# Performance work log

Measured on AMD Instinct MI355X. Metric: run time of the kernel, lower is better.

The kernel has to match this reference:

```python
import jax, jax.numpy as jnp
import numpy as np

D_M, L_OBS, ALPHA, D_H, D_V, N_HEADS = 64, 256, 256, 256, 64, 8


def setup_inputs():
    key = jax.random.key(0)
    ks = jax.random.split(key, 18)
    x_ts = jax.random.normal(ks[0], (D_M, L_OBS), dtype=jnp.float32)
    t_raw = jax.random.uniform(ks[1], (D_M, L_OBS), dtype=jnp.float32) * ALPHA
    drop = jax.random.uniform(ks[2], (D_M, L_OBS)) < 0.5
    t_ts = jnp.where(drop, -1.0, t_raw)  # negative time == invalid observation
    global_means = jax.random.normal(ks[3], (D_M,), dtype=jnp.float32)
    s = 0.05
    return {
        'x_ts': x_ts, 't_ts': t_ts, 'global_means': global_means,
        'conv_w': jax.random.normal(ks[4], (D_H, D_M)) * s,
        'conv_b': jax.random.normal(ks[5], (D_H,)) * s,
        't2v_w': jax.random.normal(ks[6], (N_HEADS, D_V)),
        't2v_phi': jax.random.normal(ks[7], (N_HEADS, D_V)),
        'wq_w': jax.random.normal(ks[8], (N_HEADS, D_V, D_V)) * s,
        'wq_b': jax.random.normal(ks[9], (N_HEADS, D_V)) * s,
        'wk_w': jax.random.normal(ks[10], (N_HEADS, D_V, D_V)) * s,
        'wk_b': jax.random.normal(ks[11], (N_HEADS, D_V)) * s,
        'proj_w': jax.random.normal(ks[12], (D_H, N_HEADS)) * s,
        'proj_b': jax.random.normal(ks[13], (D_H,)) * s,
        'g1_w': jax.random.normal(ks[14], (D_H, 2 * D_H)) * s,
        'g1_b': jax.random.normal(ks[15], (D_H,)) * s,
        'g2_w': jax.random.normal(ks[16], (D_H, D_H)) * s,
        'g2_b': jax.random.normal(ks[17], (D_H,)) * s,
    }


def _time2vec(tau, w, phi):
    # tau [...], w/phi [H, D_V] -> [H, *tau.shape, D_V]; dim 0 linear, rest sin
    shp = (N_HEADS,) + (1,) * tau.ndim + (D_V,)
    full = w.reshape(shp) * tau[None, ..., None] + phi.reshape(shp)
    return jnp.concatenate([full[..., :1], jnp.sin(full[..., 1:])], axis=-1)


def _impute_row(x, t, gm):
    # ALPHA grid via int(time), then forward-fill starting from global mean.
    valid = (~jnp.isnan(x)) & (t >= 0)
    idx = t.astype(jnp.int32)  # truncation matches int(obs_time.item()) for t>=0
    inr = valid & (idx < ALPHA)
    seg = jnp.where(inr, idx, ALPHA)  # invalid obs go to dropped segment
    order = jnp.arange(L_OBS, dtype=jnp.int32)
    last = jax.ops.segment_max(jnp.where(inr, order, -1), seg,
                               num_segments=ALPHA + 1)[:ALPHA]
    present = last >= 0
    vals = x[jnp.clip(last, 0, L_OBS - 1)]          # value written to each slot
    pos = jnp.where(present, jnp.arange(ALPHA, dtype=jnp.int32), -1)
    lastpos = jax.lax.cummax(pos, axis=0)            # last observed slot <= t
    return jnp.where(lastpos >= 0, vals[jnp.clip(lastpos, 0, ALPHA - 1)], gm)


def _forward(x_ts, t_ts, global_means, conv_w, conv_b, t2v_w, t2v_phi,
             wq_w, wq_b, wk_w, wk_b, proj_w, proj_b, g1_w, g1_b, g2_w, g2_b):
    # --- imputation branch ---
    regular = jax.vmap(_impute_row)(x_ts, t_ts, global_means)  # [d_m, alpha]
    e_imp = (conv_w @ regular).T + conv_b                      # [alpha, d_h]
    # --- mTAND branch (masked attention over ragged observations) ---
    valid = (~jnp.isnan(x_ts)) & (t_ts >= 0)                   # [d_m, L]
    x_safe = jnp.where(valid, x_ts, 0.0)
    t_safe = jnp.where(valid, t_ts, 0.0)
    alpha_pts = jnp.arange(ALPHA, dtype=jnp.float32)
    theta_a = _time2vec(alpha_pts, t2v_w, t2v_phi)             # [H, alpha, d_v]
    q = jnp.einsum('had,hed->hae', theta_a, wq_w) + wq_b[:, None, :]
    theta_o = _time2vec(t_safe, t2v_w, t2v_phi)                # [H, d_m, L, d_v]
    k = jnp.einsum('hjld,hed->hjle', theta_o, wk_w) + wk_b[:, None, None, :]
    scores = jnp.einsum('hae,hjle->hjal', q, k) / np.float32(np.sqrt(D_V))
    scores = jnp.where(valid[None, :, None, :], scores, -1e9)  # exp underflows to 0
    attn = jax.nn.softmax(scores, axis=-1)                     # [H, d_m, alpha, L]
    # fully-invalid features: uniform attn * x_safe==0 -> zeros (matches torch)
    interp = jnp.einsum('hjal,jl->jah', attn, x_safe)          # [d_m, alpha, H]
    e_attn = (interp @ proj_w.T + proj_b).mean(axis=0)         # [alpha, d_h]
    # --- hidden_space gate ---
    concat = jnp.concatenate([e_imp, e_attn], axis=-1)         # [alpha, 2*d_h]
    g = jax.nn.sigmoid(jax.nn.relu(concat @ g1_w.T + g1_b) @ g2_w.T + g2_b)
    return g * e_imp + (1.0 - g) * e_attn                      # [alpha, d_h]


def reference(x_ts, t_ts, global_means, conv_w, conv_b, t2v_w, t2v_phi,
              wq_w, wq_b, wk_w, wk_b, proj_w, proj_b, g1_w, g1_b, g2_w, g2_b):
    return _forward(x_ts, t_ts, global_means, conv_w, conv_b, t2v_w, t2v_phi,
                    wq_w, wq_b, wk_w, wk_b, proj_w, proj_b, g1_w, g1_b, g2_w, g2_b)
```

## Files before the change

### kernel.cpp

```cpp
#include <hip/hip_runtime.h>

#define D_M     64
#define L_OBS   256
#define ALPHA   256
#define D_H     256
#define D_V     64
#define N_HEADS 8

typedef _Float16 half8 __attribute__((ext_vector_type(8)));
typedef float    f32x4 __attribute__((ext_vector_type(4)));

__global__ __launch_bounds__(256) void prep_kernel(
    const float* __restrict__ x_ts, const float* __restrict__ t_ts,
    const float* __restrict__ gm,
    const float* __restrict__ t2v_w, const float* __restrict__ t2v_phi,
    const float* __restrict__ wq_w, const float* __restrict__ wq_b,
    const float* __restrict__ wk_w,
    float* __restrict__ regular, float* __restrict__ QWbuf,
    float* __restrict__ QWabsG)
{
    const int tid = threadIdx.x;

    __shared__ int   last[ALPHA];
    __shared__ float vals[ALPHA];
    __shared__ int   wtot[4];
    __shared__ __align__(16) float wq_s[D_V][68];
    __shared__ __align__(16) float thA[16][68];
    __shared__ __align__(16) float QaT[16][68];

    if (blockIdx.x < D_M) {
        const int m  = blockIdx.x;
        const int l  = tid;
        const int wv = tid >> 6;
        const int ln = tid & 63;
        last[l] = -1;
        __syncthreads();
        float x = x_ts[m * L_OBS + l];
        float t = t_ts[m * L_OBS + l];
        bool valid = (x == x) && (t >= 0.0f);
        int idx = (int)t;
        if (valid && idx < ALPHA) atomicMax(&last[idx], l);
        __syncthreads();
        int li = last[l];
        vals[l] = (li >= 0) ? x_ts[m * L_OBS + li] : 0.0f;
        int p = (li >= 0) ? l : -1;
        #pragma unroll
        for (int s = 1; s < 64; s <<= 1) {
            int q = __shfl_up(p, s);
            if (ln >= s && q > p) p = q;
        }
        if (ln == 63) wtot[wv] = p;
        __syncthreads();
        int pre = -1;
        for (int w = 0; w < 4; w++)
            if (w < wv && wtot[w] > pre) pre = wtot[w];
        int lp = (pre > p) ? pre : p;
        regular[m * ALPHA + l] = (lp >= 0) ? vals[lp] : gm[m];
    } else {
        const int pb = blockIdx.x - D_M;
        const int h  = pb >> 4;
        const int a0 = (pb & 15) * 16;

        {
            const float4* w4 = (const float4*)(wq_w + h * D_V * D_V);
            #pragma unroll
            for (int i = 0; i < 4; i++) {
                int f = i * 256 + tid;
                float4 v = w4[f];
                int e = f >> 4, c = (f & 15) * 4;
                *(float4*)&wq_s[e][c] = v;
            }
        }
        {
            int al = tid >> 4, j0 = (tid & 15) * 4;
            float tv = (float)(a0 + al);
            #pragma unroll
            for (int j = 0; j < 4; j++) {
                int d = j0 + j;
                float f = t2v_w[h * D_V + d] * tv + t2v_phi[h * D_V + d];
                thA[al][d] = (d == 0) ? f : __sinf(f);
            }
        }
        __syncthreads();

        {
            const int e  = tid >> 2;
            const int ap = tid & 3;
            float accA[4] = {0.f, 0.f, 0.f, 0.f};
            const float4* wrow = (const float4*)&wq_s[e][0];
            #pragma unroll
            for (int j = 0; j < 16; j++) {
                float4 w = wrow[j];
                #pragma unroll
                for (int k = 0; k < 4; k++) {
                    float4 tv = *(const float4*)&thA[ap + 4 * k][j * 4];
                    accA[k] += w.x * tv.x + w.y * tv.y + w.z * tv.z + w.w * tv.w;
                }
            }
            float bq = wq_b[h * D_V + e];
            #pragma unroll
            for (int k = 0; k < 4; k++) QaT[ap + 4 * k][e] = accA[k] + bq;
        }
        __syncthreads();

        const int d  = tid >> 2;
        const int ap = tid & 3;
        float accB[4] = {0.f, 0.f, 0.f, 0.f};
        #pragma unroll 4
        for (int e4 = 0; e4 < 16; e4++) {
            const float* wkp = &wk_w[(h * D_V + e4 * 4) * D_V + d];
            float w0 = wkp[0];
            float w1 = wkp[D_V];
            float w2 = wkp[2 * D_V];
            float w3 = wkp[3 * D_V];
            #pragma unroll
            for (int k = 0; k < 4; k++) {
                float4 qv = *(const float4*)&QaT[ap + 4 * k][e4 * 4];
                accB[k] += qv.x * w0 + qv.y * w1 + qv.z * w2 + qv.w * w3;
            }
        }
        #pragma unroll
        for (int k = 0; k < 4; k++)
            QWbuf[h * D_V * ALPHA + d * ALPHA + a0 + ap + 4 * k] = accB[k];

        __syncthreads();
        #pragma unroll
        for (int k = 0; k < 4; k++)
            wq_s[d][ap + 4 * k] = (d == 0) ? 0.0f : fabsf(accB[k]);
        __syncthreads();
        if (tid < 16) {
            float s = 0.0f;
            #pragma unroll 8
            for (int dd = 0; dd < D_V; dd++) s += wq_s[dd][tid];
            QWabsG[h * ALPHA + a0 + tid] = s;
        }
    }
}

__global__ __launch_bounds__(256) void attn_mfma_kernel(
    const float* __restrict__ x_ts, const float* __restrict__ t_ts,
    const float* __restrict__ t2v_w, const float* __restrict__ t2v_phi,
    const float* __restrict__ QWbuf, const float* __restrict__ QWabsG,
    float* __restrict__ interp)
{
    const int m   = blockIdx.x;
    const int h   = blockIdx.y;
    const int tid = threadIdx.x;
    const int wv  = tid >> 6;
    const int ln  = tid & 63;
    const int lg  = ln >> 4;
    const int lc  = ln & 15;

    __shared__ float t_sh[L_OBS], x_sh[L_OBS], mk_sh[L_OBS];
    __shared__ float w_sh[D_V], phi_sh[D_V];
    __shared__ __align__(16) _Float16 hiB[1024];
    __shared__ __align__(16) _Float16 reB[1024];
    __shared__ float red_s[8];

    {
        float x = x_ts[m * L_OBS + tid];
        float t = t_ts[m * L_OBS + tid];
        bool v = (x == x) && (t >= 0.0f);
        x_sh[tid]  = v ? x : 0.0f;
        t_sh[tid]  = v ? t : 0.0f;
        mk_sh[tid] = v ? 0.0f : -1.0e9f;
        float tmx = v ? t : -3.0e38f;
        float tmn = v ? t : 3.0e38f;
        #pragma unroll
        for (int s = 1; s < 64; s <<= 1) {
            tmx = fmaxf(tmx, __shfl_xor(tmx, s));
            tmn = fminf(tmn, __shfl_xor(tmn, s));
        }
        if (ln == 0) { red_s[wv] = tmx; red_s[4 + wv] = tmn; }
    }
    if (tid < D_V)          w_sh[tid]         = t2v_w[h * D_V + tid];
    else if (tid < 2 * D_V) phi_sh[tid - D_V] = t2v_phi[h * D_V + tid - D_V];
    __syncthreads();

    const float tmaxv = fmaxf(fmaxf(red_s[0], red_s[1]), fmaxf(red_s[2], red_s[3]));
    const float tminv = fminf(fminf(red_s[4], red_s[5]), fminf(red_s[6], red_s[7]));
    const bool  anyv  = tmaxv > -1.0e37f;

    const float* __restrict__ QWh = QWbuf + h * D_V * ALPHA;
    const float w0 = w_sh[0], p0 = phi_sh[0];
    const float SCALE2 = 0.18033688011112042f;

    half8 ahf[4][2], arf[4][2];
    float qw0[4][4], sB[4][4];
    #pragma unroll
    for (int at = 0; at < 4; at++) {
        const int abase = wv * 64 + at * 16;
        const int arowA = abase + lc;
        #pragma unroll
        for (int kb = 0; kb < 2; kb++) {
            #pragma unroll
            for (int j = 0; j < 8; j++) {
                int d = 1 + kb * 32 + ((j >> 2) << 4) + (lg << 2) + (j & 3);
                float q = (d < D_V) ? QWh[d * ALPHA + arowA] : 0.0f;
                _Float16 qh = (_Float16)q;
                ahf[at][kb][j] = qh;
                arf[at][kb][j] = (_Float16)(q - (float)qh);
            }
        }
        const int arowD = abase + lg * 4;
        #pragma unroll
        for (int r = 0; r < 4; r++) {
            float q0 = QWh[arowD + r];
            qw0[at][r] = q0;
            float u = q0 * w0;
            float lin = q0 * p0 + fmaxf(u * tmaxv, u * tminv);
            sB[at][r] = SCALE2 * (lin + QWabsG[h * ALPHA + arowD + r]);
        }
    }

    float ssum[4][4], axs[4][4];
    #pragma unroll
    for (int at = 0; at < 4; at++)
        #pragma unroll
        for (int r = 0; r < 4; r++) { ssum[at][r] = 0.0f; axs[at][r] = 0.0f; }

    const int wc  = tid >> 5;
    const int lcw = (tid >> 1) & 15;
    const int dB  = 1 + (wc >> 2) * 32 + (wc & 3) * 4 + ((tid & 1) << 4);

    for (int lt = 0; lt < 16; lt++) {
        if (lt) __syncthreads();
        {
            float tvw = t_sh[lt * 16 + lcw];
            float s0 = __sinf(fmaf(w_sh[(dB + 0) & 63], tvw, phi_sh[(dB + 0) & 63]));
            float s1 = __sinf(fmaf(w_sh[(dB + 1) & 63], tvw, phi_sh[(dB + 1) & 63]));
            float s2 = __sinf(fmaf(w_sh[(dB + 2) & 63], tvw, phi_sh[(dB + 2) & 63]));
            float s3 = __sinf(fmaf(w_sh[(dB + 3) & 63], tvw, phi_sh[(dB + 3) & 63]));
            union { _Float16 hv[4]; float2 f2; } hw, rw;
            hw.hv[0] = (_Float16)s0; hw.hv[1] = (_Float16)s1;
            hw.hv[2] = (_Float16)s2; hw.hv[3] = (_Float16)s3;
            rw.hv[0] = (_Float16)(s0 - (float)hw.hv[0]);
            rw.hv[1] = (_Float16)(s1 - (float)hw.hv[1]);
            rw.hv[2] = (_Float16)(s2 - (float)hw.hv[2]);
            rw.hv[3] = (_Float16)(s3 - (float)hw.hv[3]);
            *(float2*)&hiB[tid * 4] = hw.f2;
            *(float2*)&reB[tid * 4] = rw.f2;
        }
        __syncthreads();
        const int l = lt * 16 + lc;
        const float tv  = t_sh[l];
        const float xv  = x_sh[l];
        const float mkv = mk_sh[l];
        const float tau = fmaf(w0, tv, p0);

        half8 bh[2], br[2];
        #pragma unroll
        for (int kb = 0; kb < 2; kb++) {
            int fi = ((kb * 4 + lg) * 16 + lc) * 8;
            bh[kb] = *(const half8*)&hiB[fi];
            br[kb] = *(const half8*)&reB[fi];
        }

        #pragma unroll
        for (int at = 0; at < 4; at++) {
            f32x4 acc;
            #pragma unroll
            for (int r = 0; r < 4; r++) acc[r] = qw0[at][r] * tau;
            #pragma unroll
            for (int kb = 0; kb < 2; kb++) {
                acc = __builtin_amdgcn_mfma_f32_16x16x32_f16(ahf[at][kb], bh[kb], acc, 0, 0, 0);
                acc = __builtin_amdgcn_mfma_f32_16x16x32_f16(ahf[at][kb], br[kb], acc, 0, 0, 0);
                acc = __builtin_amdgcn_mfma_f32_16x16x32_f16(arf[at][kb], bh[kb], acc, 0, 0, 0);
            }
            #pragma unroll
            for (int r = 0; r < 4; r++) {
                float p = __builtin_amdgcn_exp2f(fmaf(acc[r], SCALE2, mkv) - sB[at][r]);
                ssum[at][r] += p;
                axs[at][r]   = fmaf(p, xv, axs[at][r]);
            }
        }
    }

    #pragma unroll
    for (int at = 0; at < 4; at++) {
        #pragma unroll
        for (int r = 0; r < 4; r++) {
            float S = ssum[at][r];
            float A = axs[at][r];
            S += __shfl_xor(S, 1); A += __shfl_xor(A, 1);
            S += __shfl_xor(S, 2); A += __shfl_xor(A, 2);
            S += __shfl_xor(S, 4); A += __shfl_xor(A, 4);
            S += __shfl_xor(S, 8); A += __shfl_xor(A, 8);
            if (lc == 0) {
                int a = wv * 64 + at * 16 + lg * 4 + r;
                interp[a * (D_M * N_HEADS) + m * N_HEADS + h] =
                    anyv ? (A / S) : 0.0f;
            }
        }
    }
}

__global__ __launch_bounds__(256) void final_kernel(
    const float* __restrict__ regular, const float* __restrict__ interp,
    const float* __restrict__ conv_w, const float* __restrict__ conv_b,
    const float* __restrict__ proj_w, const float* __restrict__ proj_b,
    const float* __restrict__ g1_w, const float* __restrict__ g1_b,
    const float* __restrict__ g2_w, const float* __restrict__ g2_b,
    float* __restrict__ out)
{
    const int a = blockIdx.x;
    const int tid = threadIdx.x;
    __shared__ float isum_s[N_HEADS];
    __shared__ __align__(16) float col[D_M];
    __shared__ __align__(16) float c_s[2 * D_H];
    __shared__ __align__(16) float h_s[D_H];

    if (tid < 64) {
        const float4* i4 = (const float4*)&interp[a * (D_M * N_HEADS) + tid * 8];
        float4 v0 = i4[0], v1 = i4[1];
        float v[8] = {v0.x, v0.y, v0.z, v0.w, v1.x, v1.y, v1.z, v1.w};
        #pragma unroll
        for (int s = 1; s < 64; s <<= 1) {
            #pragma unroll
            for (int j = 0; j < 8; j++) v[j] += __shfl_xor(v[j], s);
        }
        if (tid == 0) {
            #pragma unroll
            for (int j = 0; j < 8; j++) isum_s[j] = v[j];
        }
    } else if (tid < 128) {
        col[tid - 64] = regular[(tid - 64) * ALPHA + a];
    }
    __syncthreads();

    float vattn;
    {
        const float4* p4 = (const float4*)&proj_w[tid * N_HEADS];
        float4 v0 = p4[0], v1 = p4[1];
        float sum = v0.x * isum_s[0] + v0.y * isum_s[1] + v0.z * isum_s[2]
                  + v0.w * isum_s[3] + v1.x * isum_s[4] + v1.y * isum_s[5]
                  + v1.z * isum_s[6] + v1.w * isum_s[7];
        vattn = proj_b[tid] + sum * (1.0f / 64.0f);
    }
    float vimp;
    {
        const float4* row = (const float4*)&conv_w[tid * D_M];
        const float4* c4  = (const float4*)col;
        float s0 = 0.f, s1 = 0.f, s2 = 0.f, s3 = 0.f;
        #pragma unroll
        for (int i = 0; i < D_M / 4; i++) {
            float4 r = row[i]; float4 c = c4[i];
            s0 += r.x * c.x; s1 += r.y * c.y; s2 += r.z * c.z; s3 += r.w * c.w;
        }
        vimp = conv_b[tid] + ((s0 + s1) + (s2 + s3));
    }
    c_s[tid]       = vimp;
    c_s[D_H + tid] = vattn;
    __syncthreads();

    {
        const float4* grow = (const float4*)&g1_w[tid * 2 * D_H];
        const float4* c4 = (const float4*)c_s;
        float s0 = 0.f, s1 = 0.f, s2 = 0.f, s3 = 0.f;
        #pragma unroll 8
        for (int i = 0; i < (2 * D_H) / 4; i++) {
            float4 g = grow[i]; float4 c = c4[i];
            s0 += g.x * c.x; s1 += g.y * c.y; s2 += g.z * c.z; s3 += g.w * c.w;
        }
        float hid = g1_b[tid] + ((s0 + s1) + (s2 + s3));
        h_s[tid] = fmaxf(hid, 0.0f);
    }
    __syncthreads();
    {
        const float4* grow = (const float4*)&g2_w[tid * D_H];
        const float4* h4 = (const float4*)h_s;
        float s0 = 0.f, s1 = 0.f, s2 = 0.f, s3 = 0.f;
        #pragma unroll 8
        for (int i = 0; i < D_H / 4; i++) {
            float4 g = grow[i]; float4 hh = h4[i];
            s0 += g.x * hh.x; s1 += g.y * hh.y; s2 += g.z * hh.z; s3 += g.w * hh.w;
        }
        float z = g2_b[tid] + ((s0 + s1) + (s2 + s3));
        float gate = 1.0f / (1.0f + __expf(-z));
        out[a * D_H + tid] = gate * vimp + (1.0f - gate) * vattn;
    }
}

extern "C" void kernel_launch(void* const* d_in, const int* in_sizes, int n_in,
                              void* d_out, int out_size, void* d_ws, size_t ws_size,
                              hipStream_t stream)
{
    (void)in_sizes; (void)n_in; (void)out_size; (void)ws_size;

    const float* x_ts    = (const float*)d_in[0];
    const float* t_ts    = (const float*)d_in[1];
    const float* gm      = (const float*)d_in[2];
    const float* conv_w  = (const float*)d_in[3];
    const float* conv_b  = (const float*)d_in[4];
    const float* t2v_w   = (const float*)d_in[5];
    const float* t2v_phi = (const float*)d_in[6];
    const float* wq_w    = (const float*)d_in[7];
    const float* wq_b    = (const float*)d_in[8];
    const float* wk_w    = (const float*)d_in[9];
    const float* proj_w  = (const float*)d_in[11];
    const float* proj_b  = (const float*)d_in[12];
    const float* g1_w    = (const float*)d_in[13];
    const float* g1_b    = (const float*)d_in[14];
    const float* g2_w    = (const float*)d_in[15];
    const float* g2_b    = (const float*)d_in[16];

    float* out = (float*)d_out;

    float* ws      = (float*)d_ws;
    float* regular = ws;
    float* QWbuf   = regular + D_M * ALPHA;
    float* interp  = QWbuf + N_HEADS * D_V * ALPHA;
    float* QWabs   = interp + ALPHA * D_M * N_HEADS;

    prep_kernel<<<D_M + 128, 256, 0, stream>>>(
        x_ts, t_ts, gm, t2v_w, t2v_phi, wq_w, wq_b, wk_w,
        regular, QWbuf, QWabs);
    attn_mfma_kernel<<<dim3(D_M, N_HEADS), 256, 0, stream>>>(
        x_ts, t_ts, t2v_w, t2v_phi, QWbuf, QWabs, interp);
    final_kernel<<<ALPHA, 256, 0, stream>>>(
        regular, interp, conv_w, conv_b, proj_w, proj_b,
        g1_w, g1_b, g2_w, g2_b, out);
}
```

Baseline: 60.89 us.

## Split attention over observation halves with double-buffered fragments and partial-sum merge

The attention kernel grid gains a dimension that splits the 256 observations into two halves. This doubles the block count from 512 to 1024 so more of the GPU is used. Each block writes partial numerator and denominator sums, and the final kernel adds the two halves and divides. The time2vec fragment staging is double-buffered so the next tile's sin values are computed while the current tile's MFMAs run, leaving one barrier per iteration. The softmax shift constant is also folded into the accumulator's initial value. In exchange the workspace grows and the final kernel reads more data.

```diff
diff --git a/kernel.cpp b/kernel.cpp
--- a/kernel.cpp
+++ b/kernel.cpp
@@ -141,10 +141,11 @@
     const float* __restrict__ x_ts, const float* __restrict__ t_ts,
     const float* __restrict__ t2v_w, const float* __restrict__ t2v_phi,
     const float* __restrict__ QWbuf, const float* __restrict__ QWabsG,
-    float* __restrict__ interp)
+    float* __restrict__ pA, float* __restrict__ pS)
 {
-    const int m   = blockIdx.x;
-    const int h   = blockIdx.y;
+    const int lh  = blockIdx.x;
+    const int m   = blockIdx.y;
+    const int h   = blockIdx.z;
     const int tid = threadIdx.x;
     const int wv  = tid >> 6;
     const int ln  = tid & 63;
@@ -153,8 +154,8 @@
 
     __shared__ float t_sh[L_OBS], x_sh[L_OBS], mk_sh[L_OBS];
     __shared__ float w_sh[D_V], phi_sh[D_V];
-    __shared__ __align__(16) _Float16 hiB[1024];
-    __shared__ __align__(16) _Float16 reB[1024];
+    __shared__ __align__(16) _Float16 hiB[2048];
+    __shared__ __align__(16) _Float16 reB[2048];
     __shared__ float red_s[8];
 
     {
@@ -179,14 +180,13 @@
 
     const float tmaxv = fmaxf(fmaxf(red_s[0], red_s[1]), fmaxf(red_s[2], red_s[3]));
     const float tminv = fminf(fminf(red_s[4], red_s[5]), fminf(red_s[6], red_s[7]));
-    const bool  anyv  = tmaxv > -1.0e37f;
 
     const float* __restrict__ QWh = QWbuf + h * D_V * ALPHA;
     const float w0 = w_sh[0], p0 = phi_sh[0];
     const float SCALE2 = 0.18033688011112042f;
 
     half8 ahf[4][2], arf[4][2];
-    float qw0[4][4], sB[4][4];
+    float qw0[4][4], c0b[4][4];
     #pragma unroll
     for (int at = 0; at < 4; at++) {
         const int abase = wv * 64 + at * 16;
@@ -209,7 +209,7 @@
             qw0[at][r] = q0;
             float u = q0 * w0;
             float lin = q0 * p0 + fmaxf(u * tmaxv, u * tminv);
-            sB[at][r] = SCALE2 * (lin + QWabsG[h * ALPHA + arowD + r]);
+            c0b[at][r] = -(lin + QWabsG[h * ALPHA + arowD + r]);
         }
     }
 
@@ -223,44 +223,50 @@
     const int lcw = (tid >> 1) & 15;
     const int dB  = 1 + (wc >> 2) * 32 + (wc & 3) * 4 + ((tid & 1) << 4);
 
-    for (int lt = 0; lt < 16; lt++) {
-        if (lt) __syncthreads();
-        {
-            float tvw = t_sh[lt * 16 + lcw];
-            float s0 = __sinf(fmaf(w_sh[(dB + 0) & 63], tvw, phi_sh[(dB + 0) & 63]));
-            float s1 = __sinf(fmaf(w_sh[(dB + 1) & 63], tvw, phi_sh[(dB + 1) & 63]));
-            float s2 = __sinf(fmaf(w_sh[(dB + 2) & 63], tvw, phi_sh[(dB + 2) & 63]));
-            float s3 = __sinf(fmaf(w_sh[(dB + 3) & 63], tvw, phi_sh[(dB + 3) & 63]));
-            union { _Float16 hv[4]; float2 f2; } hw, rw;
-            hw.hv[0] = (_Float16)s0; hw.hv[1] = (_Float16)s1;
-            hw.hv[2] = (_Float16)s2; hw.hv[3] = (_Float16)s3;
-            rw.hv[0] = (_Float16)(s0 - (float)hw.hv[0]);
-            rw.hv[1] = (_Float16)(s1 - (float)hw.hv[1]);
-            rw.hv[2] = (_Float16)(s2 - (float)hw.hv[2]);
-            rw.hv[3] = (_Float16)(s3 - (float)hw.hv[3]);
-            *(float2*)&hiB[tid * 4] = hw.f2;
-            *(float2*)&reB[tid * 4] = rw.f2;
-        }
-        __syncthreads();
+    auto write_frags = [&](int lt, int buf) {
+        float tvw = t_sh[lt * 16 + lcw];
+        float s0 = __sinf(fmaf(w_sh[(dB + 0) & 63], tvw, phi_sh[(dB + 0) & 63]));
+        float s1 = __sinf(fmaf(w_sh[(dB + 1) & 63], tvw, phi_sh[(dB + 1) & 63]));
+        float s2 = __sinf(fmaf(w_sh[(dB + 2) & 63], tvw, phi_sh[(dB + 2) & 63]));
+        float s3 = __sinf(fmaf(w_sh[(dB + 3) & 63], tvw, phi_sh[(dB + 3) & 63]));
+        union { _Float16 hv[4]; float2 f2; } hw, rw;
+        hw.hv[0] = (_Float16)s0; hw.hv[1] = (_Float16)s1;
+        hw.hv[2] = (_Float16)s2; hw.hv[3] = (_Float16)s3;
+        rw.hv[0] = (_Float16)(s0 - (float)hw.hv[0]);
+        rw.hv[1] = (_Float16)(s1 - (float)hw.hv[1]);
+        rw.hv[2] = (_Float16)(s2 - (float)hw.hv[2]);
+        rw.hv[3] = (_Float16)(s3 - (float)hw.hv[3]);
+        *(float2*)&hiB[buf * 1024 + tid * 4] = hw.f2;
+        *(float2*)&reB[buf * 1024 + tid * 4] = rw.f2;
+    };
+
+    write_frags(lh * 8, 0);
+    __syncthreads();
+
+    for (int i = 0; i < 8; i++) {
+        const int lt  = lh * 8 + i;
+        const int cur = i & 1;
+        half8 bh[2], br[2];
+        #pragma unroll
+        for (int kb = 0; kb < 2; kb++) {
+            int fi = cur * 1024 + ((kb * 4 + lg) * 16 + lc) * 8;
+            bh[kb] = *(const half8*)&hiB[fi];
+            br[kb] = *(const half8*)&reB[fi];
+        }
+        if (i < 7) write_frags(lt + 1, cur ^ 1);
+
         const int l = lt * 16 + lc;
         const float tv  = t_sh[l];
         const float xv  = x_sh[l];
         const float mkv = mk_sh[l];
         const float tau = fmaf(w0, tv, p0);
 
-        half8 bh[2], br[2];
-        #pragma unroll
-        for (int kb = 0; kb < 2; kb++) {
-            int fi = ((kb * 4 + lg) * 16 + lc) * 8;
-            bh[kb] = *(const half8*)&hiB[fi];
-            br[kb] = *(const half8*)&reB[fi];
-        }
-
         #pragma unroll
         for (int at = 0; at < 4; at++) {
             f32x4 acc;
             #pragma unroll
-            for (int r = 0; r < 4; r++) acc[r] = qw0[at][r] * tau;
+            for (int r = 0; r < 4; r++)
+                acc[r] = fmaf(qw0[at][r], tau, c0b[at][r]);
             #pragma unroll
             for (int kb = 0; kb < 2; kb++) {
                 acc = __builtin_amdgcn_mfma_f32_16x16x32_f16(ahf[at][kb], bh[kb], acc, 0, 0, 0);
@@ -269,11 +275,12 @@
             }
             #pragma unroll
             for (int r = 0; r < 4; r++) {
-                float p = __builtin_amdgcn_exp2f(fmaf(acc[r], SCALE2, mkv) - sB[at][r]);
+                float p = __builtin_amdgcn_exp2f(fmaf(acc[r], SCALE2, mkv));
                 ssum[at][r] += p;
                 axs[at][r]   = fmaf(p, xv, axs[at][r]);
             }
         }
+        __syncthreads();
     }
 
     #pragma unroll
@@ -288,15 +295,18 @@
             S += __shfl_xor(S, 8); A += __shfl_xor(A, 8);
             if (lc == 0) {
                 int a = wv * 64 + at * 16 + lg * 4 + r;
-                interp[a * (D_M * N_HEADS) + m * N_HEADS + h] =
-                    anyv ? (A / S) : 0.0f;
+                int idx = lh * (ALPHA * D_M * N_HEADS)
+                        + a * (D_M * N_HEADS) + m * N_HEADS + h;
+                pA[idx] = A;
+                pS[idx] = S;
             }
         }
     }
 }
 
 __global__ __launch_bounds__(256) void final_kernel(
-    const float* __restrict__ regular, const float* __restrict__ interp,
+    const float* __restrict__ regular,
+    const float* __restrict__ pA, const float* __restrict__ pS,
     const float* __restrict__ conv_w, const float* __restrict__ conv_b,
     const float* __restrict__ proj_w, const float* __restrict__ proj_b,
     const float* __restrict__ g1_w, const float* __restrict__ g1_b,
@@ -305,15 +315,27 @@
 {
     const int a = blockIdx.x;
     const int tid = threadIdx.x;
+    const int HALF = ALPHA * D_M * N_HEADS;
     __shared__ float isum_s[N_HEADS];
     __shared__ __align__(16) float col[D_M];
     __shared__ __align__(16) float c_s[2 * D_H];
     __shared__ __align__(16) float h_s[D_H];
 
     if (tid < 64) {
-        const float4* i4 = (const float4*)&interp[a * (D_M * N_HEADS) + tid * 8];
-        float4 v0 = i4[0], v1 = i4[1];
-        float v[8] = {v0.x, v0.y, v0.z, v0.w, v1.x, v1.y, v1.z, v1.w};
+        int base = a * (D_M * N_HEADS) + tid * 8;
+        const float4* a04 = (const float4*)&pA[base];
+        const float4* a14 = (const float4*)&pA[HALF + base];
+        const float4* s04 = (const float4*)&pS[base];
+        const float4* s14 = (const float4*)&pS[HALF + base];
+        float4 A0 = a04[0], A1 = a04[1], B0 = a14[0], B1 = a14[1];
+        float4 S0 = s04[0], S1 = s04[1], T0 = s14[0], T1 = s14[1];
+        float Av[8] = {A0.x + B0.x, A0.y + B0.y, A0.z + B0.z, A0.w + B0.w,
+                       A1.x + B1.x, A1.y + B1.y, A1.z + B1.z, A1.w + B1.w};
+        float Sv[8] = {S0.x + T0.x, S0.y + T0.y, S0.z + T0.z, S0.w + T0.w,
+                       S1.x + T1.x, S1.y + T1.y, S1.z + T1.z, S1.w + T1.w};
+        float v[8];
+        #pragma unroll
+        for (int j = 0; j < 8; j++) v[j] = (Sv[j] > 0.0f) ? (Av[j] / Sv[j]) : 0.0f;
         #pragma unroll
         for (int s = 1; s < 64; s <<= 1) {
             #pragma unroll
@@ -409,15 +431,16 @@
     float* ws      = (float*)d_ws;
     float* regular = ws;
     float* QWbuf   = regular + D_M * ALPHA;
-    float* interp  = QWbuf + N_HEADS * D_V * ALPHA;
-    float* QWabs   = interp + ALPHA * D_M * N_HEADS;
+    float* pA      = QWbuf + N_HEADS * D_V * ALPHA;
+    float* pS      = pA + 2 * ALPHA * D_M * N_HEADS;
+    float* QWabs   = pS + 2 * ALPHA * D_M * N_HEADS;
 
     prep_kernel<<<D_M + 128, 256, 0, stream>>>(
         x_ts, t_ts, gm, t2v_w, t2v_phi, wq_w, wq_b, wk_w,
         regular, QWbuf, QWabs);
-    attn_mfma_kernel<<<dim3(D_M, N_HEADS), 256, 0, stream>>>(
-        x_ts, t_ts, t2v_w, t2v_phi, QWbuf, QWabs, interp);
+    attn_mfma_kernel<<<dim3(2, D_M, N_HEADS), 256, 0, stream>>>(
+        x_ts, t_ts, t2v_w, t2v_phi, QWbuf, QWabs, pA, pS);
     final_kernel<<<ALPHA, 256, 0, stream>>>(
-        regular, interp, conv_w, conv_b, proj_w, proj_b,
+        regular, pA, pS, conv_w, conv_b, proj_w, proj_b,
         g1_w, g1_b, g2_w, g2_b, out);
 }
```

Result: slower. 75.33 us (+23.7%).

## Split attention over alpha halves, double-buffer sin fragments, fold bias into accumulator

Applied to the files above, without the earlier changes.

Doubles the attention kernel grid by splitting the 256 alpha rows into two blocks of 128, so 1024 blocks run instead of 512 on a GPU with many CUs. Each block recomputes the sin fragments and the validity reductions, which duplicates that work. The B-fragment LDS buffer is double-buffered so the next tile's sin values are written while the current tile's MFMAs run, leaving one barrier per iteration instead of two. The softmax shift is folded into the accumulator's initial value, removing one subtract per score.

```diff
diff --git a/kernel.cpp b/kernel.cpp
--- a/kernel.cpp
+++ b/kernel.cpp
@@ -143,8 +143,9 @@
     const float* __restrict__ QWbuf, const float* __restrict__ QWabsG,
     float* __restrict__ interp)
 {
-    const int m   = blockIdx.x;
-    const int h   = blockIdx.y;
+    const int ah  = blockIdx.x;
+    const int m   = blockIdx.y;
+    const int h   = blockIdx.z;
     const int tid = threadIdx.x;
     const int wv  = tid >> 6;
     const int ln  = tid & 63;
@@ -153,8 +154,8 @@
 
     __shared__ float t_sh[L_OBS], x_sh[L_OBS], mk_sh[L_OBS];
     __shared__ float w_sh[D_V], phi_sh[D_V];
-    __shared__ __align__(16) _Float16 hiB[1024];
-    __shared__ __align__(16) _Float16 reB[1024];
+    __shared__ __align__(16) _Float16 hiB[2048];
+    __shared__ __align__(16) _Float16 reB[2048];
     __shared__ float red_s[8];
 
     {
@@ -185,11 +186,11 @@
     const float w0 = w_sh[0], p0 = phi_sh[0];
     const float SCALE2 = 0.18033688011112042f;
 
-    half8 ahf[4][2], arf[4][2];
-    float qw0[4][4], sB[4][4];
+    half8 ahf[2][2], arf[2][2];
+    float qw0[2][4], c0b[2][4];
     #pragma unroll
-    for (int at = 0; at < 4; at++) {
-        const int abase = wv * 64 + at * 16;
+    for (int at = 0; at < 2; at++) {
+        const int abase = ah * 128 + wv * 32 + at * 16;
         const int arowA = abase + lc;
         #pragma unroll
         for (int kb = 0; kb < 2; kb++) {
@@ -209,13 +210,13 @@
             qw0[at][r] = q0;
             float u = q0 * w0;
             float lin = q0 * p0 + fmaxf(u * tmaxv, u * tminv);
-            sB[at][r] = SCALE2 * (lin + QWabsG[h * ALPHA + arowD + r]);
-        }
-    }
-
-    float ssum[4][4], axs[4][4];
+            c0b[at][r] = -(lin + QWabsG[h * ALPHA + arowD + r]);
+        }
+    }
+
+    float ssum[2][4], axs[2][4];
     #pragma unroll
-    for (int at = 0; at < 4; at++)
+    for (int at = 0; at < 2; at++)
         #pragma unroll
         for (int r = 0; r < 4; r++) { ssum[at][r] = 0.0f; axs[at][r] = 0.0f; }
 
@@ -223,44 +224,49 @@
     const int lcw = (tid >> 1) & 15;
     const int dB  = 1 + (wc >> 2) * 32 + (wc & 3) * 4 + ((tid & 1) << 4);
 
+    auto write_frags = [&](int lt, int buf) {
+        float tvw = t_sh[lt * 16 + lcw];
+        float s0 = __sinf(fmaf(w_sh[(dB + 0) & 63], tvw, phi_sh[(dB + 0) & 63]));
+        float s1 = __sinf(fmaf(w_sh[(dB + 1) & 63], tvw, phi_sh[(dB + 1) & 63]));
+        float s2 = __sinf(fmaf(w_sh[(dB + 2) & 63], tvw, phi_sh[(dB + 2) & 63]));
+        float s3 = __sinf(fmaf(w_sh[(dB + 3) & 63], tvw, phi_sh[(dB + 3) & 63]));
+        union { _Float16 hv[4]; float2 f2; } hw, rw;
+        hw.hv[0] = (_Float16)s0; hw.hv[1] = (_Float16)s1;
+        hw.hv[2] = (_Float16)s2; hw.hv[3] = (_Float16)s3;
+        rw.hv[0] = (_Float16)(s0 - (float)hw.hv[0]);
+        rw.hv[1] = (_Float16)(s1 - (float)hw.hv[1]);
+        rw.hv[2] = (_Float16)(s2 - (float)hw.hv[2]);
+        rw.hv[3] = (_Float16)(s3 - (float)hw.hv[3]);
+        *(float2*)&hiB[buf * 1024 + tid * 4] = hw.f2;
+        *(float2*)&reB[buf * 1024 + tid * 4] = rw.f2;
+    };
+
+    write_frags(0, 0);
+    __syncthreads();
+
     for (int lt = 0; lt < 16; lt++) {
-        if (lt) __syncthreads();
-        {
-            float tvw = t_sh[lt * 16 + lcw];
-            float s0 = __sinf(fmaf(w_sh[(dB + 0) & 63], tvw, phi_sh[(dB + 0) & 63]));
-            float s1 = __sinf(fmaf(w_sh[(dB + 1) & 63], tvw, phi_sh[(dB + 1) & 63]));
-            float s2 = __sinf(fmaf(w_sh[(dB + 2) & 63], tvw, phi_sh[(dB + 2) & 63]));
-            float s3 = __sinf(fmaf(w_sh[(dB + 3) & 63], tvw, phi_sh[(dB + 3) & 63]));
-            union { _Float16 hv[4]; float2 f2; } hw, rw;
-            hw.hv[0] = (_Float16)s0; hw.hv[1] = (_Float16)s1;
-            hw.hv[2] = (_Float16)s2; hw.hv[3] = (_Float16)s3;
-            rw.hv[0] = (_Float16)(s0 - (float)hw.hv[0]);
-            rw.hv[1] = (_Float16)(s1 - (float)hw.hv[1]);
-            rw.hv[2] = (_Float16)(s2 - (float)hw.hv[2]);
-            rw.hv[3] = (_Float16)(s3 - (float)hw.hv[3]);
-            *(float2*)&hiB[tid * 4] = hw.f2;
-            *(float2*)&reB[tid * 4] = rw.f2;
-        }
-        __syncthreads();
+        const int cur = lt & 1;
+        half8 bh[2], br[2];
+        #pragma unroll
+        for (int kb = 0; kb < 2; kb++) {
+            int fi = cur * 1024 + ((kb * 4 + lg) * 16 + lc) * 8;
+            bh[kb] = *(const half8*)&hiB[fi];
+            br[kb] = *(const half8*)&reB[fi];
+        }
+        if (lt < 15) write_frags(lt + 1, cur ^ 1);
+
         const int l = lt * 16 + lc;
         const float tv  = t_sh[l];
         const float xv  = x_sh[l];
         const float mkv = mk_sh[l];
         const float tau = fmaf(w0, tv, p0);
 
-        half8 bh[2], br[2];
-        #pragma unroll
-        for (int kb = 0; kb < 2; kb++) {
-            int fi = ((kb * 4 + lg) * 16 + lc) * 8;
-            bh[kb] = *(const half8*)&hiB[fi];
-            br[kb] = *(const half8*)&reB[fi];
-        }
-
-        #pragma unroll
-        for (int at = 0; at < 4; at++) {
+        #pragma unroll
+        for (int at = 0; at < 2; at++) {
             f32x4 acc;
             #pragma unroll
-            for (int r = 0; r < 4; r++) acc[r] = qw0[at][r] * tau;
+            for (int r = 0; r < 4; r++)
+                acc[r] = fmaf(qw0[at][r], tau, c0b[at][r]);
             #pragma unroll
             for (int kb = 0; kb < 2; kb++) {
                 acc = __builtin_amdgcn_mfma_f32_16x16x32_f16(ahf[at][kb], bh[kb], acc, 0, 0, 0);
@@ -269,15 +275,16 @@
             }
             #pragma unroll
             for (int r = 0; r < 4; r++) {
-                float p = __builtin_amdgcn_exp2f(fmaf(acc[r], SCALE2, mkv) - sB[at][r]);
+                float p = __builtin_amdgcn_exp2f(fmaf(acc[r], SCALE2, mkv));
                 ssum[at][r] += p;
                 axs[at][r]   = fmaf(p, xv, axs[at][r]);
             }
         }
+        __syncthreads();
     }
 
     #pragma unroll
-    for (int at = 0; at < 4; at++) {
+    for (int at = 0; at < 2; at++) {
         #pragma unroll
         for (int r = 0; r < 4; r++) {
             float S = ssum[at][r];
@@ -287,7 +294,7 @@
             S += __shfl_xor(S, 4); A += __shfl_xor(A, 4);
             S += __shfl_xor(S, 8); A += __shfl_xor(A, 8);
             if (lc == 0) {
-                int a = wv * 64 + at * 16 + lg * 4 + r;
+                int a = ah * 128 + wv * 32 + at * 16 + lg * 4 + r;
                 interp[a * (D_M * N_HEADS) + m * N_HEADS + h] =
                     anyv ? (A / S) : 0.0f;
             }
@@ -415,7 +422,7 @@
     prep_kernel<<<D_M + 128, 256, 0, stream>>>(
         x_ts, t_ts, gm, t2v_w, t2v_phi, wq_w, wq_b, wk_w,
         regular, QWbuf, QWabs);
-    attn_mfma_kernel<<<dim3(D_M, N_HEADS), 256, 0, stream>>>(
+    attn_mfma_kernel<<<dim3(2, D_M, N_HEADS), 256, 0, stream>>>(
         x_ts, t_ts, t2v_w, t2v_phi, QWbuf, QWabs, interp);
     final_kernel<<<ALPHA, 256, 0, stream>>>(
         regular, interp, conv_w, conv_b, proj_w, proj_b,
```

Result: faster. 57.59 us (-5.4%).
